# Optimization experiments

Measured on AMD Instinct MI355X. Metric: run time of the kernel, lower is better.

Reference implementation:

```python
import jax, jax.numpy as jnp
import numpy as np

THETA = 10000.0
NUM_HEADS = 16
MAX_SEQ_LEN = 2048

def _rope_tables(d_k, max_seq_len, theta=THETA):
    dims = jnp.arange(0, d_k, 2, dtype=jnp.float32)
    freqs = 1.0 / theta ** (dims / d_k)
    t = jnp.arange(max_seq_len, dtype=jnp.float32)
    angles = jnp.outer(t, freqs)  # (max_seq_len, d_k//2)
    return jnp.cos(angles), jnp.sin(angles)

def _apply_rope(x, token_positions, cos_tab, sin_tab):
    # x: (..., seq_len, d_k)
    cos = jnp.repeat(cos_tab[token_positions], 2, axis=-1)  # (seq_len, d_k)
    sin = jnp.repeat(sin_tab[token_positions], 2, axis=-1)
    # interleaved rotate-half: (-x1, x0, -x3, x2, ...)
    xp = x.reshape(*x.shape[:-1], -1, 2)
    x_neg = jnp.stack([-xp[..., 1], xp[..., 0]], axis=-1).reshape(x.shape)
    return x * cos + x_neg * sin

def setup_inputs() -> dict:
    key = jax.random.key(0)
    ks = jax.random.split(key, 5)
    B, S, D = 4, 2048, 1024
    scale = 1.0 / np.sqrt(D)
    return {
        "x": jax.random.normal(ks[0], (B, S, D), dtype=jnp.float32),
        "q_proj": jax.random.normal(ks[1], (D, D), dtype=jnp.float32) * scale,
        "k_proj": jax.random.normal(ks[2], (D, D), dtype=jnp.float32) * scale,
        "v_proj": jax.random.normal(ks[3], (D, D), dtype=jnp.float32) * scale,
        "o_proj": jax.random.normal(ks[4], (D, D), dtype=jnp.float32) * scale,
        "token_positions": jnp.arange(S, dtype=jnp.int64),
    }

def reference(x, q_proj, k_proj, v_proj, o_proj, token_positions):
    B, S, D = x.shape
    H = NUM_HEADS
    d_k = D // H
    cos_tab, sin_tab = _rope_tables(d_k, MAX_SEQ_LEN)

    q = (x @ q_proj).reshape(B, S, H, d_k).transpose(0, 2, 1, 3)  # (B,H,S,d_k)
    k = (x @ k_proj).reshape(B, S, H, d_k).transpose(0, 2, 1, 3)
    v = (x @ v_proj).reshape(B, S, H, d_k).transpose(0, 2, 1, 3)

    q = _apply_rope(q, token_positions, cos_tab, sin_tab)
    k = _apply_rope(k, token_positions, cos_tab, sin_tab)

    scores = jnp.einsum('bhqd,bhkd->bhqk', q, k) / jnp.sqrt(jnp.float32(d_k))
    causal = jnp.tril(jnp.ones((S, S), dtype=bool))
    scores = jnp.where(causal, scores, -jnp.inf)
    attn = jax.nn.softmax(scores, axis=-1)
    out = jnp.einsum('bhqk,bhkd->bhqd', attn, v)  # (B,H,S,d_k)
    out = out.transpose(0, 2, 1, 3).reshape(B, S, D)
    return out @ o_proj
```

## Files before the change

### kernel.cpp

```cpp
#include <hip/hip_runtime.h>
#include <hip/hip_bf16.h>
#include <stdint.h>


typedef __attribute__((ext_vector_type(8))) short short8;
typedef __attribute__((ext_vector_type(4))) float floatx4;
typedef __attribute__((ext_vector_type(16))) float floatx16;

#define MFMA16(a,b,c) __builtin_amdgcn_mfma_f32_16x16x32_bf16((a),(b),(c),0,0,0)
#define MFMA32(a,b,c) __builtin_amdgcn_mfma_f32_32x32x16_bf16((a),(b),(c),0,0,0)
#define BAR() __builtin_amdgcn_s_barrier()
#define LGKM0 asm volatile("s_waitcnt lgkmcnt(0)" ::: "memory")
#define VMCNT6 asm volatile("s_waitcnt vmcnt(6)" ::: "memory")

__device__ __forceinline__ uint32_t fbits(float f){ uint32_t u; __builtin_memcpy(&u,&f,4); return u; }
__device__ __forceinline__ unsigned short f2bf(float f) {
    uint32_t u = fbits(f);
    return (unsigned short)((u + 0x7fffu + ((u>>16)&1u)) >> 16);
}
__device__ __forceinline__ float bf2f(unsigned short s){ uint32_t u = (uint32_t)s<<16; float f; __builtin_memcpy(&f,&u,4); return f; }
__device__ __forceinline__ uint32_t pkbf(float lo, float hi) {
#if __has_builtin(__builtin_amdgcn_cvt_pk_bf16_f32)
    auto r = __builtin_amdgcn_cvt_pk_bf16_f32(lo, hi);
    uint32_t u; __builtin_memcpy(&u, &r, sizeof(u));
    return u;
#else
    return __builtin_amdgcn_perm(fbits(hi)+0x8000u, fbits(lo)+0x8000u, 0x07060302u);
#endif
}

__device__ __forceinline__ void load_lds16(const unsigned short* g, unsigned short* l) {
    __builtin_amdgcn_global_load_lds(
        (const __attribute__((address_space(1))) void*)g,
        (__attribute__((address_space(3))) void*)l, 16, 0, 0);
}

__device__ __forceinline__ bool sniff_f32(const unsigned short* xr) {
    int lane = threadIdx.x & 63;
    int bad = 0;
#pragma unroll
    for (int i = 0; i < 16; i++) {
        float v = bf2f(xr[lane * 16 + i]);
        if (!(__builtin_fabsf(v) < 1e10f)) bad = 1;
    }
    return __ballot(bad != 0) != 0ull;
}

__global__ __launch_bounds__(256) void prep_k(
    const void* __restrict__ x,
    const void* __restrict__ wq, const void* __restrict__ wk,
    const void* __restrict__ wv, const void* __restrict__ wo,
    unsigned short* __restrict__ WT, unsigned short* __restrict__ WoT,
    float2* __restrict__ tab, unsigned short* __restrict__ xb) {
    int blk = blockIdx.x, t = threadIdx.x;
    bool f32 = sniff_f32((const unsigned short*)x);
    if (blk < 4096) {
        __shared__ unsigned short tile[32][33];
        int mat = blk >> 10, r = blk & 1023;
        const void* src = (mat == 0) ? wq : (mat == 1) ? wk : (mat == 2) ? wv : wo;
        unsigned short* dst = (mat < 3) ? (WT + (size_t)mat * 1048576) : WoT;
        int bx = (r & 31) * 32, by = (r >> 5) * 32;
        int tx = t & 31, ty = t >> 5;
#pragma unroll
        for (int j = 0; j < 32; j += 8) {
            size_t idx = (size_t)(by + ty + j) * 1024 + bx + tx;
            float v = f32 ? ((const float*)src)[idx] : bf2f(((const unsigned short*)src)[idx]);
            tile[ty + j][tx] = f2bf(v);
        }
        __syncthreads();
#pragma unroll
        for (int j = 0; j < 32; j += 8)
            dst[(size_t)(bx + ty + j) * 1024 + by + tx] = tile[tx][ty + j];
    } else if (blk < 4352) {
        int i = (blk - 4096) * 256 + t;
        int pos = i >> 5, j = i & 31;
        float freq = exp2f(-(float)(2 * j) * (1.0f / 64.0f) * 13.287712379549449f);
        float a = (float)pos * freq;
        tab[i] = make_float2(cosf(a), sinf(a));
    } else {
        size_t base = (size_t)(blk - 4352) * 2048 + (size_t)t * 8;
        if (f32) {
            const float4* s4 = (const float4*)((const float*)x + base);
            float4 a = s4[0], b = s4[1];
            uint4 o;
            o.x = pkbf(a.x, a.y); o.y = pkbf(a.z, a.w);
            o.z = pkbf(b.x, b.y); o.w = pkbf(b.z, b.w);
            *(uint4*)(xb + base) = o;
        } else {
            *(uint4*)(xb + base) = *(const uint4*)((const unsigned short*)x + base);
        }
    }
}

template <int MODE>
__global__ __launch_bounds__(512, 2) void gemm8(
    const unsigned short* __restrict__ A,
    const unsigned short* __restrict__ Bt,
    void* __restrict__ C0,
    unsigned short* __restrict__ C1,
    unsigned short* __restrict__ C2,
    const float2* __restrict__ tab,
    const unsigned short* __restrict__ xsniff) {
    const int K = 1024;
    extern __shared__ __align__(16) char smraw[];
    unsigned short* Asm = (unsigned short*)smraw;
    unsigned short* Bsm = Asm + 3 * 8192;

    int t = threadIdx.x;
    int lane = t & 63, w = t >> 6;
    int quad = lane >> 4, l15 = lane & 15;
    int wm = (w >> 2) * 64, wn = (w & 3) * 64;

    int nbx = gridDim.x;
    int flat = blockIdx.y * nbx + blockIdx.x;
    int cpx = (nbx * gridDim.y) >> 3;
    int swzid = (flat & 7) * cpx + (flat >> 3);
    int bx = swzid % nbx, by = swzid / nbx;
    int m0 = by * 128, n0 = bx * 256;

    floatx4 acc[4][4];
#pragma unroll
    for (int i = 0; i < 4; i++)
#pragma unroll
        for (int j = 0; j < 4; j++) acc[i][j] = (floatx4){0.f, 0.f, 0.f, 0.f};

    int srow = t >> 3;
    int sg = ((t & 7) ^ (srow & 7)) * 8;
    const unsigned short* gA = A + (size_t)(m0 + srow) * K + sg;
    const unsigned short* gB = Bt + (size_t)(n0 + srow) * K + sg;
    unsigned short* lA = Asm + w * 512;
    unsigned short* lB = Bsm + w * 512;

    int rA[4], rB[4], ce[2];
#pragma unroll
    for (int m = 0; m < 4; m++) rA[m] = (wm + m * 16 + l15) * 64;
#pragma unroll
    for (int n = 0; n < 4; n++) rB[n] = (wn + n * 16 + l15) * 64;
#pragma unroll
    for (int ks = 0; ks < 2; ks++)
        ce[ks] = ((ks * 64 + quad * 16) ^ ((l15 & 7) << 4)) >> 1;

#pragma unroll
    for (int kt = 0; kt < 2; kt++) {
#pragma unroll
        for (int h = 0; h < 2; h++)
            load_lds16(gA + (size_t)h * 64 * K + kt * 64, lA + kt * 8192 + h * 4096);
#pragma unroll
        for (int c = 0; c < 4; c++)
            load_lds16(gB + (size_t)c * 64 * K + kt * 64, lB + kt * 16384 + c * 4096);
    }
    VMCNT6;
    __syncthreads();

    int cur = 0, nxt = 2;
#pragma unroll 1
    for (int kt = 0; kt < 16; kt++) {
        const unsigned short* cA = Asm + cur * 8192;
        const unsigned short* cB = Bsm + cur * 16384;
        unsigned short* nA = lA + nxt * 8192;
        unsigned short* nB = lB + nxt * 16384;
        size_t ko = (size_t)(kt + 2) * 64;
        short8 a0[4], a1[4], bf0, bf1;

#pragma unroll
        for (int m = 0; m < 4; m++) a0[m] = *(const short8*)(cA + rA[m] + ce[0]);
        bf0 = *(const short8*)(cB + rB[0] + ce[0]);
        bf1 = *(const short8*)(cB + rB[1] + ce[0]);
        load_lds16(gA + ko, nA);
        load_lds16(gA + (size_t)64 * K + ko, nA + 4096);
        BAR(); LGKM0;
        __builtin_amdgcn_s_setprio(1);
#pragma unroll
        for (int m = 0; m < 4; m++) {
            acc[m][0] = MFMA16(a0[m], bf0, acc[m][0]);
            acc[m][1] = MFMA16(a0[m], bf1, acc[m][1]);
        }
        __builtin_amdgcn_s_setprio(0);
        BAR();

        bf0 = *(const short8*)(cB + rB[2] + ce[0]);
        bf1 = *(const short8*)(cB + rB[3] + ce[0]);
        load_lds16(gB + ko, nB);
        load_lds16(gB + (size_t)64 * K + ko, nB + 4096);
        BAR(); LGKM0;
        __builtin_amdgcn_s_setprio(1);
#pragma unroll
        for (int m = 0; m < 4; m++) {
            acc[m][2] = MFMA16(a0[m], bf0, acc[m][2]);
            acc[m][3] = MFMA16(a0[m], bf1, acc[m][3]);
        }
        __builtin_amdgcn_s_setprio(0);
        BAR();

#pragma unroll
        for (int m = 0; m < 4; m++) a1[m] = *(const short8*)(cA + rA[m] + ce[1]);
        bf0 = *(const short8*)(cB + rB[0] + ce[1]);
        bf1 = *(const short8*)(cB + rB[1] + ce[1]);
        load_lds16(gB + (size_t)128 * K + ko, nB + 8192);
        load_lds16(gB + (size_t)192 * K + ko, nB + 12288);
        BAR(); LGKM0;
        __builtin_amdgcn_s_setprio(1);
#pragma unroll
        for (int m = 0; m < 4; m++) {
            acc[m][0] = MFMA16(a1[m], bf0, acc[m][0]);
            acc[m][1] = MFMA16(a1[m], bf1, acc[m][1]);
        }
        __builtin_amdgcn_s_setprio(0);
        BAR();

        bf0 = *(const short8*)(cB + rB[2] + ce[1]);
        bf1 = *(const short8*)(cB + rB[3] + ce[1]);
        BAR(); LGKM0;
        __builtin_amdgcn_s_setprio(1);
#pragma unroll
        for (int m = 0; m < 4; m++) {
            acc[m][2] = MFMA16(a1[m], bf0, acc[m][2]);
            acc[m][3] = MFMA16(a1[m], bf1, acc[m][3]);
        }
        __builtin_amdgcn_s_setprio(0);
        VMCNT6;
        BAR();

        cur = (cur == 2) ? 0 : cur + 1;
        nxt = (nxt == 2) ? 0 : nxt + 1;
    }

    bool out_f32 = (MODE == 0) ? sniff_f32(xsniff) : false;
#pragma unroll
    for (int i = 0; i < 4; i++) {
#pragma unroll
        for (int j = 0; j < 4; j++) {
            int col = n0 + wn + j * 16 + l15;
            int row0 = m0 + wm + i * 16 + quad * 4;
            if (MODE == 0) {
#pragma unroll
                for (int r = 0; r < 4; r++) {
                    size_t idx = (size_t)(row0 + r) * 1024 + col;
                    if (out_f32) ((float*)C0)[idx] = acc[i][j][r];
                    else ((unsigned short*)C0)[idx] = f2bf(acc[i][j][r]);
                }
            } else {
                int which = col >> 10, nn = col & 1023;
                int b = row0 >> 11, s0 = row0 & 2047;
                if (which == 2) {
                    int hh = nn >> 6, d = nn & 63;
                    uint32_t lo = pkbf(acc[i][j][0], acc[i][j][1]);
                    uint32_t hi = pkbf(acc[i][j][2], acc[i][j][3]);
                    *(uint64_t*)(C2 + ((size_t)((b * 16 + hh) * 64 + d)) * 2048 + s0) =
                        (uint64_t)lo | ((uint64_t)hi << 32);
                } else {
                    int d = nn & 63;
                    unsigned short* dst = (which == 0) ? (unsigned short*)C0 : C1;
                    float sc = (which == 0) ? 0.18033688011112042f : 1.0f;
#pragma unroll
                    for (int r = 0; r < 4; r++) {
                        int s = s0 + r;
                        float v = acc[i][j][r];
                        float pv = __shfl_xor(v, 1);
                        float2 cs = tab[(s << 5) + (d >> 1)];
                        float o = (d & 1) ? (v * cs.x + pv * cs.y) : (v * cs.x - pv * cs.y);
                        dst[((size_t)(b * 2048 + s)) * 1024 + nn] = f2bf(o * sc);
                    }
                }
            }
        }
    }
}

__global__ __launch_bounds__(256, 4) void flash_k(
    const unsigned short* __restrict__ Qb,
    const unsigned short* __restrict__ Kb,
    const unsigned short* __restrict__ Vt,
    unsigned short* __restrict__ A2) {
    __shared__ __align__(16) unsigned short Kl[2][64 * 64];
    __shared__ __align__(16) unsigned short Vl[2][64 * 64];

    int bh = blockIdx.x;
    int y = blockIdx.y;
    int qt = (y < 8) ? (15 - y) : (y - 8);
    int b = bh >> 4, h = bh & 15;
    int t = threadIdx.x, lane = t & 63, w = t >> 6;
    int l31 = lane & 31, half = lane >> 5;
    size_t base = ((size_t)b * 2048) * 1024 + h * 64;
    int q0w = qt * 128 + w * 32;

    short8 Qf[4];
#pragma unroll
    for (int ks = 0; ks < 4; ks++)
        Qf[ks] = *(const short8*)(Qb + base + (size_t)(q0w + l31) * 1024 + ks * 16 + half * 8);

    floatx16 O[2];
    O[0] = (floatx16)0.0f; O[1] = (floatx16)0.0f;
    float lsum = 0.f;

    int nk = 2 * (qt + 1);

    int srow = t >> 2;
    const unsigned short* kg = Kb + base + (size_t)srow * 1024 + (t & 3) * 16;
    const unsigned short* vg = Vt + ((size_t)(bh * 64 + srow)) * 2048 + (t & 3) * 16;
    int sw0 = srow * 64 + ((((t & 3) * 2 + 0) ^ (srow & 7)) * 8);
    int sw1 = srow * 64 + ((((t & 3) * 2 + 1) ^ (srow & 7)) * 8);

    short8 rk0 = *(const short8*)(kg);
    short8 rk1 = *(const short8*)(kg + 8);
    short8 rv0 = *(const short8*)(vg);
    short8 rv1 = *(const short8*)(vg + 8);

    for (int kt = 0; kt < nk; kt++) {
        int k0 = kt * 64, bf = kt & 1;
        *(short8*)&Kl[bf][sw0] = rk0;
        *(short8*)&Kl[bf][sw1] = rk1;
        *(short8*)&Vl[bf][sw0] = rv0;
        *(short8*)&Vl[bf][sw1] = rv1;
        __syncthreads();
        if (kt + 1 < nk) {
            size_t ko = (size_t)(kt + 1) * 64;
            rk0 = *(const short8*)(kg + ko * 1024);
            rk1 = *(const short8*)(kg + ko * 1024 + 8);
            rv0 = *(const short8*)(vg + ko);
            rv1 = *(const short8*)(vg + ko + 8);
        }
#pragma unroll
        for (int mb = 0; mb < 2; mb++) {
            if (k0 + mb * 32 >= q0w + 32) continue;
            short8 Ka[4];
#pragma unroll
            for (int ks = 0; ks < 4; ks++)
                Ka[ks] = *(const short8*)&Kl[bf][(mb * 32 + l31) * 64 +
                                                 (((ks * 2 + half) ^ (l31 & 7)) * 8)];
            floatx16 Sc = (floatx16)0.0f;
#pragma unroll
            for (int ks = 0; ks < 4; ks++)
                Sc = MFMA32(Ka[ks], Qf[ks], Sc);

            bool domask = (k0 + mb * 32 + 31 > q0w);
            float p[16];
#pragma unroll
            for (int e = 0; e < 16; e++) {
                float v = exp2f(Sc[e]);
                if (domask) {
                    int kv = k0 + mb * 32 + (e & 3) + ((e >> 2) << 3) + half * 4;
                    int qq = q0w + l31;
                    v = (kv > qq) ? 0.f : v;
                }
                p[e] = v;
            }
            float t0 = (p[0] + p[1]) + (p[2] + p[3]);
            float t1 = (p[4] + p[5]) + (p[6] + p[7]);
            float t2 = (p[8] + p[9]) + (p[10] + p[11]);
            float t3 = (p[12] + p[13]) + (p[14] + p[15]);
            lsum += (t0 + t1) + (t2 + t3);
            uint32_t pkm[8];
#pragma unroll
            for (int jj = 0; jj < 8; jj++)
                pkm[jj] = pkbf(p[2 * jj], p[2 * jj + 1]);

            short8 Va[2][2];
#pragma unroll
            for (int db = 0; db < 2; db++)
#pragma unroll
                for (int ks2 = 0; ks2 < 2; ks2++)
                    Va[db][ks2] = *(const short8*)&Vl[bf][(db * 32 + l31) * 64 +
                                                         ((((mb * 2 + ks2) * 2 + half) ^ (l31 & 7)) * 8)];
#pragma unroll
            for (int ks2 = 0; ks2 < 2; ks2++) {
                uint32_t p0 = pkm[4 * ks2 + 0];
                uint32_t p1 = pkm[4 * ks2 + 1];
                uint32_t p2 = pkm[4 * ks2 + 2];
                uint32_t p3 = pkm[4 * ks2 + 3];
                uint32_t u = half ? p0 : p2;
                uint32_t v2 = half ? p1 : p3;
                uint32_t ya = (uint32_t)__shfl_xor((int)u, 32);
                uint32_t yb = (uint32_t)__shfl_xor((int)v2, 32);
                union { short8 s; uint32_t q[4]; } bb;
                bb.q[0] = half ? ya : p0;
                bb.q[1] = half ? yb : p1;
                bb.q[2] = half ? p2 : ya;
                bb.q[3] = half ? p3 : yb;
#pragma unroll
                for (int db = 0; db < 2; db++)
                    O[db] = MFMA32(Va[db][ks2], bb.s, O[db]);
            }
        }
    }

    float tot = lsum + __shfl_xor(lsum, 32);
    float inv = 1.0f / tot;
#pragma unroll
    for (int db = 0; db < 2; db++) {
        int scol = q0w + l31;
        unsigned short* op = A2 + base + (size_t)scol * 1024;
#pragma unroll
        for (int g = 0; g < 4; g++) {
            int d0 = db * 32 + half * 4 + g * 8;
            float v0 = O[db][g * 4 + 0] * inv;
            float v1 = O[db][g * 4 + 1] * inv;
            float v2 = O[db][g * 4 + 2] * inv;
            float v3 = O[db][g * 4 + 3] * inv;
            uint32_t lo = pkbf(v0, v1), hi = pkbf(v2, v3);
            *(uint64_t*)(op + d0) = (uint64_t)lo | ((uint64_t)hi << 32);
        }
    }
}

extern "C" void kernel_launch(void* const* d_in, const int* in_sizes, int n_in,
                              void* d_out, int out_size, void* d_ws, size_t ws_size,
                              hipStream_t stream) {
    const void* x  = d_in[0];
    const void* wq = d_in[1];
    const void* wk = d_in[2];
    const void* wv = d_in[3];
    const void* wo = d_in[4];

    char* ws = (char*)d_ws;
    unsigned short* WT  = (unsigned short*)(ws);
    unsigned short* WoT = (unsigned short*)(ws + 6291456);
    float2*         tab = (float2*)(ws + 8388608);
    unsigned short* xb  = (unsigned short*)(ws + 8913920);
    unsigned short* Qb  = (unsigned short*)(ws + 8913920 + 16777216ull);
    unsigned short* Kb  = (unsigned short*)(ws + 8913920 + 2ull * 16777216);
    unsigned short* Vt  = (unsigned short*)(ws + 8913920 + 3ull * 16777216);
    unsigned short* A2  = xb;

    (void)hipFuncSetAttribute(reinterpret_cast<const void*>(gemm8<1>),
                              hipFuncAttributeMaxDynamicSharedMemorySize, 147456);
    (void)hipFuncSetAttribute(reinterpret_cast<const void*>(gemm8<0>),
                              hipFuncAttributeMaxDynamicSharedMemorySize, 147456);

    prep_k<<<8448, 256, 0, stream>>>(x, wq, wk, wv, wo, WT, WoT, tab, xb);

    gemm8<1><<<dim3(12, 64), 512, 147456, stream>>>(xb, WT, Qb, Kb, Vt, tab,
                                                    (const unsigned short*)x);
    flash_k<<<dim3(64, 16), 256, 0, stream>>>(Qb, Kb, Vt, A2);
    gemm8<0><<<dim3(4, 64), 512, 147456, stream>>>(A2, WoT, d_out, nullptr, nullptr, tab,
                                                   (const unsigned short*)x);
}
```

Measured before the change: 256.3 us.

## Split flash attention KV sub-blocks across two wave groups with LDS reduction

```diff
diff --git a/kernel.cpp b/kernel.cpp
--- a/kernel.cpp
+++ b/kernel.cpp
@@ -26,6 +26,13 @@
     return u;
 #else
     return __builtin_amdgcn_perm(fbits(hi)+0x8000u, fbits(lo)+0x8000u, 0x07060302u);
+#endif
+}
+__device__ __forceinline__ float fexp2(float x) {
+#if __has_builtin(__builtin_amdgcn_exp2f)
+    return __builtin_amdgcn_exp2f(x);
+#else
+    return exp2f(x);
 #endif
 }
 
@@ -267,22 +274,26 @@
     }
 }
 
-__global__ __launch_bounds__(256, 4) void flash_k(
+__global__ __launch_bounds__(512, 6) void flash_k(
     const unsigned short* __restrict__ Qb,
     const unsigned short* __restrict__ Kb,
     const unsigned short* __restrict__ Vt,
     unsigned short* __restrict__ A2) {
-    __shared__ __align__(16) unsigned short Kl[2][64 * 64];
-    __shared__ __align__(16) unsigned short Vl[2][64 * 64];
+    __shared__ __align__(16) char sm[33792];
+    unsigned short* Kl = (unsigned short*)sm;
+    unsigned short* Vl = (unsigned short*)(sm + 16384);
+    float4* Osw = (float4*)sm;
+    float*  lsw = (float*)(sm + 32768);
 
     int bh = blockIdx.x;
     int y = blockIdx.y;
     int qt = (y < 8) ? (15 - y) : (y - 8);
     int b = bh >> 4, h = bh & 15;
     int t = threadIdx.x, lane = t & 63, w = t >> 6;
+    int wq = w & 3, wg = w >> 2;
     int l31 = lane & 31, half = lane >> 5;
     size_t base = ((size_t)b * 2048) * 1024 + h * 64;
-    int q0w = qt * 128 + w * 32;
+    int q0w = qt * 128 + wq * 32;
 
     short8 Qf[4];
 #pragma unroll
@@ -295,53 +306,47 @@
 
     int nk = 2 * (qt + 1);
 
-    int srow = t >> 2;
-    const unsigned short* kg = Kb + base + (size_t)srow * 1024 + (t & 3) * 16;
-    const unsigned short* vg = Vt + ((size_t)(bh * 64 + srow)) * 2048 + (t & 3) * 16;
-    int sw0 = srow * 64 + ((((t & 3) * 2 + 0) ^ (srow & 7)) * 8);
-    int sw1 = srow * 64 + ((((t & 3) * 2 + 1) ^ (srow & 7)) * 8);
-
-    short8 rk0 = *(const short8*)(kg);
-    short8 rk1 = *(const short8*)(kg + 8);
-    short8 rv0 = *(const short8*)(vg);
-    short8 rv1 = *(const short8*)(vg + 8);
+    int srow = t >> 3, gs = t & 7;
+    const unsigned short* kg = Kb + base + (size_t)srow * 1024 + gs * 8;
+    const unsigned short* vg = Vt + ((size_t)(bh * 64 + srow)) * 2048 + gs * 8;
+    int sw = srow * 64 + ((gs ^ (srow & 7)) * 8);
+
+    short8 rk = *(const short8*)(kg);
+    short8 rv = *(const short8*)(vg);
 
     for (int kt = 0; kt < nk; kt++) {
         int k0 = kt * 64, bf = kt & 1;
-        *(short8*)&Kl[bf][sw0] = rk0;
-        *(short8*)&Kl[bf][sw1] = rk1;
-        *(short8*)&Vl[bf][sw0] = rv0;
-        *(short8*)&Vl[bf][sw1] = rv1;
+        *(short8*)&Kl[bf * 4096 + sw] = rk;
+        *(short8*)&Vl[bf * 4096 + sw] = rv;
         __syncthreads();
         if (kt + 1 < nk) {
             size_t ko = (size_t)(kt + 1) * 64;
-            rk0 = *(const short8*)(kg + ko * 1024);
-            rk1 = *(const short8*)(kg + ko * 1024 + 8);
-            rv0 = *(const short8*)(vg + ko);
-            rv1 = *(const short8*)(vg + ko + 8);
-        }
-#pragma unroll
-        for (int mb = 0; mb < 2; mb++) {
-            if (k0 + mb * 32 >= q0w + 32) continue;
+            rk = *(const short8*)(kg + ko * 1024);
+            rv = *(const short8*)(vg + ko);
+        }
+        int k0mb = k0 + wg * 32;
+        if (k0mb < q0w + 32) {
+            const unsigned short* Klb = Kl + bf * 4096;
+            const unsigned short* Vlb = Vl + bf * 4096;
             short8 Ka[4];
 #pragma unroll
             for (int ks = 0; ks < 4; ks++)
-                Ka[ks] = *(const short8*)&Kl[bf][(mb * 32 + l31) * 64 +
-                                                 (((ks * 2 + half) ^ (l31 & 7)) * 8)];
+                Ka[ks] = *(const short8*)&Klb[(wg * 32 + l31) * 64 +
+                                              (((ks * 2 + half) ^ (l31 & 7)) * 8)];
             floatx16 Sc = (floatx16)0.0f;
 #pragma unroll
             for (int ks = 0; ks < 4; ks++)
                 Sc = MFMA32(Ka[ks], Qf[ks], Sc);
 
-            bool domask = (k0 + mb * 32 + 31 > q0w);
+            bool domask = (k0mb + 31 > q0w);
+            int thr = q0w + l31 - k0mb - half * 4;
             float p[16];
 #pragma unroll
             for (int e = 0; e < 16; e++) {
-                float v = exp2f(Sc[e]);
+                float v = fexp2(Sc[e]);
                 if (domask) {
-                    int kv = k0 + mb * 32 + (e & 3) + ((e >> 2) << 3) + half * 4;
-                    int qq = q0w + l31;
-                    v = (kv > qq) ? 0.f : v;
+                    const int ce = (e & 3) + ((e >> 2) << 3);
+                    v = (ce > thr) ? 0.f : v;
                 }
                 p[e] = v;
             }
@@ -360,8 +365,8 @@
             for (int db = 0; db < 2; db++)
 #pragma unroll
                 for (int ks2 = 0; ks2 < 2; ks2++)
-                    Va[db][ks2] = *(const short8*)&Vl[bf][(db * 32 + l31) * 64 +
-                                                         ((((mb * 2 + ks2) * 2 + half) ^ (l31 & 7)) * 8)];
+                    Va[db][ks2] = *(const short8*)&Vlb[(db * 32 + l31) * 64 +
+                                                       ((((wg * 2 + ks2) * 2 + half) ^ (l31 & 7)) * 8)];
 #pragma unroll
             for (int ks2 = 0; ks2 < 2; ks2++) {
                 uint32_t p0 = pkm[4 * ks2 + 0];
@@ -384,21 +389,47 @@
         }
     }
 
-    float tot = lsum + __shfl_xor(lsum, 32);
-    float inv = 1.0f / tot;
-#pragma unroll
-    for (int db = 0; db < 2; db++) {
+    __syncthreads();
+    if (w < 4) {
+#pragma unroll
+        for (int db = 0; db < 2; db++)
+#pragma unroll
+            for (int g = 0; g < 4; g++)
+                Osw[(w * 8 + db * 4 + g) * 64 + lane] =
+                    make_float4(O[db][g * 4 + 0], O[db][g * 4 + 1],
+                                O[db][g * 4 + 2], O[db][g * 4 + 3]);
+        lsw[w * 64 + lane] = lsum;
+    }
+    __syncthreads();
+    if (w >= 4) {
+        int wp = w - 4;
+#pragma unroll
+        for (int db = 0; db < 2; db++)
+#pragma unroll
+            for (int g = 0; g < 4; g++) {
+                float4 o = Osw[(wp * 8 + db * 4 + g) * 64 + lane];
+                O[db][g * 4 + 0] += o.x;
+                O[db][g * 4 + 1] += o.y;
+                O[db][g * 4 + 2] += o.z;
+                O[db][g * 4 + 3] += o.w;
+            }
+        lsum += lsw[wp * 64 + lane];
+        float tot = lsum + __shfl_xor(lsum, 32);
+        float inv = 1.0f / tot;
         int scol = q0w + l31;
         unsigned short* op = A2 + base + (size_t)scol * 1024;
 #pragma unroll
-        for (int g = 0; g < 4; g++) {
-            int d0 = db * 32 + half * 4 + g * 8;
-            float v0 = O[db][g * 4 + 0] * inv;
-            float v1 = O[db][g * 4 + 1] * inv;
-            float v2 = O[db][g * 4 + 2] * inv;
-            float v3 = O[db][g * 4 + 3] * inv;
-            uint32_t lo = pkbf(v0, v1), hi = pkbf(v2, v3);
-            *(uint64_t*)(op + d0) = (uint64_t)lo | ((uint64_t)hi << 32);
+        for (int db = 0; db < 2; db++) {
+#pragma unroll
+            for (int g = 0; g < 4; g++) {
+                int d0 = db * 32 + half * 4 + g * 8;
+                float v0 = O[db][g * 4 + 0] * inv;
+                float v1 = O[db][g * 4 + 1] * inv;
+                float v2 = O[db][g * 4 + 2] * inv;
+                float v3 = O[db][g * 4 + 3] * inv;
+                uint32_t lo = pkbf(v0, v1), hi = pkbf(v2, v3);
+                *(uint64_t*)(op + d0) = (uint64_t)lo | ((uint64_t)hi << 32);
+            }
         }
     }
 }
@@ -431,7 +462,7 @@
 
     gemm8<1><<<dim3(12, 64), 512, 147456, stream>>>(xb, WT, Qb, Kb, Vt, tab,
                                                     (const unsigned short*)x);
-    flash_k<<<dim3(64, 16), 256, 0, stream>>>(Qb, Kb, Vt, A2);
+    flash_k<<<dim3(64, 16), 512, 0, stream>>>(Qb, Kb, Vt, A2);
     gemm8<0><<<dim3(4, 64), 512, 147456, stream>>>(A2, WoT, d_out, nullptr, nullptr, tab,
                                                    (const unsigned short*)x);
 }
```

After: 309.8 us. +20.9%, slower.
